# Performance work log

Measured on AMD Instinct MI355X. Metric: run time of the kernel, lower is better.

Reference implementation:

```python
import jax, jax.numpy as jnp
import numpy as np

N_NODES = 100000
N_EDGES = 800000
D_IN = 512
D_OUT = 512


def setup_inputs() -> dict:
    key = jax.random.key(0)
    ks = jax.random.split(key, 6)
    std = 1.0 / np.sqrt(D_OUT)
    return {
        "x": jax.random.normal(ks[0], (N_NODES, D_IN), dtype=jnp.float32),
        "adj_row": jax.random.randint(ks[1], (N_EDGES,), 0, N_NODES, dtype=jnp.int32),
        "adj_col": jax.random.randint(ks[2], (N_EDGES,), 0, N_NODES, dtype=jnp.int32),
        "adj_vals": jax.random.uniform(ks[3], (N_EDGES,), dtype=jnp.float32),
        "weight": jax.random.uniform(ks[4], (D_IN, D_OUT), minval=-std, maxval=std, dtype=jnp.float32),
        "b": jax.random.uniform(ks[5], (D_OUT,), minval=-std, maxval=std, dtype=jnp.float32),
    }


def reference(x, adj_row, adj_col, adj_vals, weight, b):
    # support = X W  : dense GEMM [N, D_in] x [D_in, D_out]
    support = jnp.matmul(x, weight)
    # output = A @ support + b, A given as COO (row, col, vals)
    gathered = adj_vals[:, None] * support[adj_col]  # [E, D_out]
    out = jax.ops.segment_sum(gathered, adj_row, num_segments=N_NODES)
    return out + b
```

## Files before the change

### kernel.cpp

```cpp
#include <hip/hip_runtime.h>
#include <hip/hip_bf16.h>
#include <stdint.h>

#define D 512
#define D4 (D / 4)
#define SB 256
#define CHUNK 256

typedef __bf16 bf16x8 __attribute__((ext_vector_type(8)));
typedef float  f32x4  __attribute__((ext_vector_type(4)));

__device__ __forceinline__ unsigned short f2bf(float f) {
    uint32_t u = __float_as_uint(f);
    uint32_t r = u + 0x7fffu + ((u >> 16) & 1u);
    return (unsigned short)(r >> 16);
}

__device__ __forceinline__ uint32_t pack2(float lo, float hi) {
    return (uint32_t)f2bf(lo) | ((uint32_t)f2bf(hi) << 16);
}

__device__ __forceinline__ float bflo(uint32_t p) {
    return __uint_as_float((p & 0x0000ffffu) << 16);
}
__device__ __forceinline__ float bfhi(uint32_t p) {
    return __uint_as_float(p & 0xffff0000u);
}

__global__ __launch_bounds__(256) void cvt_x_kernel(const float4* __restrict__ x,
                                                    uint4* __restrict__ xb,
                                                    long n8) {
    long i = (long)blockIdx.x * 256 + threadIdx.x;
    if (i >= n8) return;
    float4 a = x[i * 2];
    float4 b = x[i * 2 + 1];
    uint4 o;
    o.x = pack2(a.x, a.y);
    o.y = pack2(a.z, a.w);
    o.z = pack2(b.x, b.y);
    o.w = pack2(b.z, b.w);
    xb[i] = o;
}

__global__ __launch_bounds__(256) void cvt_w_kernel(const float* __restrict__ w,
                                                    unsigned short* __restrict__ wt) {
    __shared__ float t[32][33];
    const int tx = threadIdx.x & 31;
    const int ty = threadIdx.x >> 5;
    const int n0 = blockIdx.x * 32;
    const int k0 = blockIdx.y * 32;
#pragma unroll
    for (int i = 0; i < 4; ++i)
        t[ty + i * 8][tx] = w[(long)(k0 + ty + i * 8) * D + n0 + tx];
    __syncthreads();
#pragma unroll
    for (int i = 0; i < 4; ++i)
        wt[(long)(n0 + ty + i * 8) * D + k0 + tx] = f2bf(t[tx][ty + i * 8]);
}

__global__ __launch_bounds__(256) void zero_kernel(int* __restrict__ p, int n) {
    int i = blockIdx.x * 256 + threadIdx.x;
    if (i < n) p[i] = 0;
}

__global__ __launch_bounds__(256) void hist_kernel(const int* __restrict__ erow,
                                                   int* __restrict__ cnt, int nE) {
    int i = blockIdx.x * 256 + threadIdx.x;
    int stride = gridDim.x * 256;
    for (; i < nE; i += stride) atomicAdd(&cnt[erow[i]], 1);
}

__global__ __launch_bounds__(256) void scan_part_kernel(const int* __restrict__ cnt,
                                                        int* __restrict__ bsum, int M) {
    const int b = blockIdx.x;
    const int chunk = (M + SB - 1) / SB;
    const int lo = b * chunk;
    const int hi = min(M, lo + chunk);
    int s = 0;
    for (int i = lo + (int)threadIdx.x; i < hi; i += 256) s += cnt[i];
#pragma unroll
    for (int off = 32; off; off >>= 1) s += __shfl_down(s, off);
    __shared__ int ws[4];
    const int wv = threadIdx.x >> 6;
    if ((threadIdx.x & 63) == 0) ws[wv] = s;
    __syncthreads();
    if (threadIdx.x == 0) bsum[b] = ws[0] + ws[1] + ws[2] + ws[3];
}

__global__ __launch_bounds__(SB) void scan_base_kernel(const int* __restrict__ bsum,
                                                       int* __restrict__ bbase,
                                                       int* __restrict__ rowptr, int M) {
    const int tid  = (int)threadIdx.x;
    const int lane = tid & 63;
    const int wv   = tid >> 6;
    const int v = bsum[tid];
    int s = v;
#pragma unroll
    for (int off = 1; off < 64; off <<= 1) {
        int t = __shfl_up(s, off);
        if (lane >= off) s += t;
    }
    __shared__ int wsum[4];
    if (lane == 63) wsum[wv] = s;
    __syncthreads();
    int wb = 0;
    for (int j = 0; j < wv; ++j) wb += wsum[j];
    bbase[tid] = wb + s - v;
    if (tid == SB - 1) rowptr[M] = wb + s;
}

__global__ __launch_bounds__(256) void scan_final_kernel(const int* __restrict__ cnt,
                                                         const int* __restrict__ bbase,
                                                         int* __restrict__ rowptr,
                                                         int* __restrict__ heads, int M) {
    const int b = blockIdx.x;
    const int chunk = (M + SB - 1) / SB;
    const int lo = b * chunk;
    const int hi = min(M, lo + chunk);
    const int lane = threadIdx.x & 63;
    const int wv   = threadIdx.x >> 6;
    __shared__ int wsum[4];
    __shared__ int s_carry;
    if (threadIdx.x == 0) s_carry = bbase[b];
    __syncthreads();
    for (int base = lo; base < hi; base += 256) {
        const int i = base + (int)threadIdx.x;
        const int v = (i < hi) ? cnt[i] : 0;
        int s = v;
#pragma unroll
        for (int off = 1; off < 64; off <<= 1) {
            int t = __shfl_up(s, off);
            if (lane >= off) s += t;
        }
        if (lane == 63) wsum[wv] = s;
        __syncthreads();
        int wb = s_carry;
        for (int j = 0; j < wv; ++j) wb += wsum[j];
        const int excl = wb + s - v;
        if (i < hi) { rowptr[i] = excl; heads[i] = excl; }
        __syncthreads();
        if (threadIdx.x == 0) s_carry += wsum[0] + wsum[1] + wsum[2] + wsum[3];
        __syncthreads();
    }
}

__global__ __launch_bounds__(256) void edge_sort_kernel(const int* __restrict__ erow,
                                                        const int* __restrict__ ecol,
                                                        const float* __restrict__ eval,
                                                        int* __restrict__ heads,
                                                        int* __restrict__ scol,
                                                        float* __restrict__ sval,
                                                        int nE) {
    int i = blockIdx.x * 256 + threadIdx.x;
    int stride = gridDim.x * 256;
    for (; i < nE; i += stride) {
        const int r = erow[i];
        const int p = atomicAdd(&heads[r], 1);
        scol[p] = ecol[i];
        sval[p] = eval[i];
    }
}

__global__ __launch_bounds__(256) void gemm_kernel(const unsigned short* __restrict__ Xb,
                                                   const unsigned short* __restrict__ Wt,
                                                   unsigned short* __restrict__ Sup,
                                                   int M) {
    __shared__ __align__(16) unsigned short As[128 * 64];
    __shared__ __align__(16) unsigned short Bs[128 * 64];
    const int tid  = threadIdx.x;
    const int wv   = tid >> 6;
    const int lane = tid & 63;
    const int tileM = blockIdx.x * 128;
    const int tileN = blockIdx.y * 128;
    const int wm = wv >> 1, wn = wv & 1;

    f32x4 acc[4][4];
#pragma unroll
    for (int i = 0; i < 4; ++i)
#pragma unroll
        for (int j = 0; j < 4; ++j) acc[i][j] = (f32x4)0.0f;

    const int srow = lane >> 3;
    const int sgrn = (lane & 7) ^ srow;
    const int scol = sgrn * 8;

    const int fm  = lane & 15;
    const int fkq = lane >> 4;

    for (int kt = 0; kt < D; kt += 64) {
        __syncthreads();
#pragma unroll
        for (int i = 0; i < 4; ++i) {
            const int c   = wv * 4 + i;
            const int row = c * 8 + srow;
            int rg = tileM + row;
            rg = (rg < M) ? rg : (M - 1);
            const unsigned short* ga = Xb + (long)rg * D + kt + scol;
            __builtin_amdgcn_global_load_lds(
                (const __attribute__((address_space(1))) void*)ga,
                (__attribute__((address_space(3))) void*)(As + c * 512), 16, 0, 0);
            const unsigned short* gb = Wt + (long)(tileN + row) * D + kt + scol;
            __builtin_amdgcn_global_load_lds(
                (const __attribute__((address_space(1))) void*)gb,
                (__attribute__((address_space(3))) void*)(Bs + c * 512), 16, 0, 0);
        }
        __syncthreads();
#pragma unroll
        for (int kk = 0; kk < 2; ++kk) {
            bf16x8 af[4], bfr[4];
#pragma unroll
            for (int mi = 0; mi < 4; ++mi) {
                const int m = wm * 64 + mi * 16 + fm;
                const int g = (kk * 4 + fkq) ^ (m & 7);
                af[mi] = *(const bf16x8*)(As + m * 64 + g * 8);
            }
#pragma unroll
            for (int ni = 0; ni < 4; ++ni) {
                const int n = wn * 64 + ni * 16 + fm;
                const int g = (kk * 4 + fkq) ^ (n & 7);
                bfr[ni] = *(const bf16x8*)(Bs + n * 64 + g * 8);
            }
#pragma unroll
            for (int mi = 0; mi < 4; ++mi)
#pragma unroll
                for (int ni = 0; ni < 4; ++ni)
                    acc[mi][ni] = __builtin_amdgcn_mfma_f32_16x16x32_bf16(
                        af[mi], bfr[ni], acc[mi][ni], 0, 0, 0);
        }
    }

    const int colb = tileN + wn * 64 + fm;
#pragma unroll
    for (int mi = 0; mi < 4; ++mi) {
        const int rb = tileM + wm * 64 + mi * 16 + fkq * 4;
#pragma unroll
        for (int r = 0; r < 4; ++r) {
            const int row = rb + r;
            if (row < M) {
                unsigned short* dst = Sup + (long)row * D + colb;
#pragma unroll
                for (int ni = 0; ni < 4; ++ni)
                    dst[ni * 16] = f2bf(acc[mi][ni][r]);
            }
        }
    }
}

__global__ __launch_bounds__(256) void aggregate_kernel(const unsigned short* __restrict__ sup,
                                                        const int* __restrict__ rowptr,
                                                        const int* __restrict__ scol,
                                                        const float* __restrict__ sval,
                                                        const float* __restrict__ bias,
                                                        float* __restrict__ out,
                                                        int M, int c0) {
    const int lane = threadIdx.x & 63;
    const int row  = (int)((blockIdx.x * 256 + threadIdx.x) >> 6);
    if (row >= M) return;
    int e = rowptr[row];
    const int end = rowptr[row + 1];

    const float4 b0 = *(const float4*)(bias + c0 + lane * 4);
    float acc[4] = {b0.x, b0.y, b0.z, b0.w};

    const unsigned short* supc = sup + c0 + lane * 4;

    for (; e + 4 <= end; e += 4) {
        const int cc0 = scol[e + 0], cc1 = scol[e + 1];
        const int cc2 = scol[e + 2], cc3 = scol[e + 3];
        const float v0 = sval[e + 0], v1 = sval[e + 1];
        const float v2 = sval[e + 2], v3 = sval[e + 3];
        const uint2 p0 = *(const uint2*)(supc + (long)cc0 * D);
        const uint2 p1 = *(const uint2*)(supc + (long)cc1 * D);
        const uint2 p2 = *(const uint2*)(supc + (long)cc2 * D);
        const uint2 p3 = *(const uint2*)(supc + (long)cc3 * D);
        acc[0] += v0 * bflo(p0.x); acc[1] += v0 * bfhi(p0.x);
        acc[2] += v0 * bflo(p0.y); acc[3] += v0 * bfhi(p0.y);
        acc[0] += v1 * bflo(p1.x); acc[1] += v1 * bfhi(p1.x);
        acc[2] += v1 * bflo(p1.y); acc[3] += v1 * bfhi(p1.y);
        acc[0] += v2 * bflo(p2.x); acc[1] += v2 * bfhi(p2.x);
        acc[2] += v2 * bflo(p2.y); acc[3] += v2 * bfhi(p2.y);
        acc[0] += v3 * bflo(p3.x); acc[1] += v3 * bfhi(p3.x);
        acc[2] += v3 * bflo(p3.y); acc[3] += v3 * bfhi(p3.y);
    }
    for (; e + 2 <= end; e += 2) {
        const int cc0 = scol[e + 0], cc1 = scol[e + 1];
        const float v0 = sval[e + 0], v1 = sval[e + 1];
        const uint2 p0 = *(const uint2*)(supc + (long)cc0 * D);
        const uint2 p1 = *(const uint2*)(supc + (long)cc1 * D);
        acc[0] += v0 * bflo(p0.x); acc[1] += v0 * bfhi(p0.x);
        acc[2] += v0 * bflo(p0.y); acc[3] += v0 * bfhi(p0.y);
        acc[0] += v1 * bflo(p1.x); acc[1] += v1 * bfhi(p1.x);
        acc[2] += v1 * bflo(p1.y); acc[3] += v1 * bfhi(p1.y);
    }
    for (; e < end; ++e) {
        const int cc = scol[e];
        const float v = sval[e];
        const uint2 p = *(const uint2*)(supc + (long)cc * D);
        acc[0] += v * bflo(p.x); acc[1] += v * bfhi(p.x);
        acc[2] += v * bflo(p.y); acc[3] += v * bfhi(p.y);
    }

    *(float4*)(out + (long)row * D + c0 + lane * 4) =
        (float4){acc[0], acc[1], acc[2], acc[3]};
}

extern "C" void kernel_launch(void* const* d_in, const int* in_sizes, int n_in,
                              void* d_out, int out_size, void* d_ws, size_t ws_size,
                              hipStream_t stream) {
    const float* x        = (const float*)d_in[0];
    const int*   adj_row  = (const int*)d_in[1];
    const int*   adj_col  = (const int*)d_in[2];
    const float* adj_vals = (const float*)d_in[3];
    const float* weight   = (const float*)d_in[4];
    const float* bias     = (const float*)d_in[5];
    float* out = (float*)d_out;

    const int M = in_sizes[0] / D;
    const int E = in_sizes[1];

    char* ws = (char*)d_ws;
    size_t off = 0;
    unsigned short* Xb  = (unsigned short*)(ws + off); off += (size_t)M * D * 2;
    unsigned short* Sup = (unsigned short*)(ws + off); off += (size_t)M * D * 2;
    unsigned short* Wt  = (unsigned short*)(ws + off); off += (size_t)D * D * 2;
    int*   rowptr = (int*)(ws + off);   off += (size_t)(M + 1) * 4;
    int*   heads  = (int*)(ws + off);   off += (size_t)M * 4;
    int*   scol   = (int*)(ws + off);   off += (size_t)E * 4;
    float* sval   = (float*)(ws + off); off += (size_t)E * 4;
    int*   bsum   = (int*)(ws + off);   off += (size_t)SB * 4;
    int*   bbase  = (int*)(ws + off);   off += (size_t)SB * 4;
    int* cnt = heads;

    zero_kernel<<<(M + 255) / 256, 256, 0, stream>>>(cnt, M);
    hist_kernel<<<1024, 256, 0, stream>>>(adj_row, cnt, E);
    scan_part_kernel<<<SB, 256, 0, stream>>>(cnt, bsum, M);
    scan_base_kernel<<<1, SB, 0, stream>>>(bsum, bbase, rowptr, M);
    scan_final_kernel<<<SB, 256, 0, stream>>>(cnt, bbase, rowptr, heads, M);
    edge_sort_kernel<<<1024, 256, 0, stream>>>(adj_row, adj_col, adj_vals,
                                               heads, scol, sval, E);

    {
        long n8 = (long)M * D / 8;
        cvt_x_kernel<<<(int)((n8 + 255) / 256), 256, 0, stream>>>(
            (const float4*)x, (uint4*)Xb, n8);
    }
    cvt_w_kernel<<<dim3(D / 32, D / 32), 256, 0, stream>>>(weight, Wt);
    gemm_kernel<<<dim3((M + 127) / 128, D / 128), 256, 0, stream>>>(Xb, Wt, Sup, M);

    aggregate_kernel<<<(M * 64 + 255) / 256, 256, 0, stream>>>(
        Sup, rowptr, scol, sval, bias, out, M, 0);
    aggregate_kernel<<<(M * 64 + 255) / 256, 256, 0, stream>>>(
        Sup, rowptr, scol, sval, bias, out, M, CHUNK);
}
```

Measured before the change: 649.0 us.

## Fuse fp32-to-bf16 X conversion into GEMM with full-width N tiles

Removes the separate X conversion kernel and its bf16 workspace buffer. The GEMM now reads fp32 X directly, converts it to bf16 in registers and stores it to LDS. Each block covers 64 rows and all 512 output columns with 8 waves, so X is read once instead of once per N tile. This cuts a full write and read of the converted X, but the A-tile path is now synchronous register loads rather than direct global-to-LDS loads, and each block holds a larger B tile in LDS (64 KB), which limits occupancy.

```diff
diff --git a/kernel.cpp b/kernel.cpp
--- a/kernel.cpp
+++ b/kernel.cpp
@@ -3,9 +3,9 @@
 #include <stdint.h>
 
 #define D 512
-#define D4 (D / 4)
 #define SB 256
 #define CHUNK 256
+#define BM 64
 
 typedef __bf16 bf16x8 __attribute__((ext_vector_type(8)));
 typedef float  f32x4  __attribute__((ext_vector_type(4)));
@@ -25,21 +25,6 @@
 }
 __device__ __forceinline__ float bfhi(uint32_t p) {
     return __uint_as_float(p & 0xffff0000u);
-}
-
-__global__ __launch_bounds__(256) void cvt_x_kernel(const float4* __restrict__ x,
-                                                    uint4* __restrict__ xb,
-                                                    long n8) {
-    long i = (long)blockIdx.x * 256 + threadIdx.x;
-    if (i >= n8) return;
-    float4 a = x[i * 2];
-    float4 b = x[i * 2 + 1];
-    uint4 o;
-    o.x = pack2(a.x, a.y);
-    o.y = pack2(a.z, a.w);
-    o.z = pack2(b.x, b.y);
-    o.w = pack2(b.z, b.w);
-    xb[i] = o;
 }
 
 __global__ __launch_bounds__(256) void cvt_w_kernel(const float* __restrict__ w,
@@ -161,18 +146,16 @@
     }
 }
 
-__global__ __launch_bounds__(256) void gemm_kernel(const unsigned short* __restrict__ Xb,
-                                                   const unsigned short* __restrict__ Wt,
-                                                   unsigned short* __restrict__ Sup,
-                                                   int M) {
-    __shared__ __align__(16) unsigned short As[128 * 64];
-    __shared__ __align__(16) unsigned short Bs[128 * 64];
+__global__ __launch_bounds__(512, 4) void gemm_kernel(const float* __restrict__ X,
+                                                      const unsigned short* __restrict__ Wt,
+                                                      unsigned short* __restrict__ Sup,
+                                                      int M) {
+    __shared__ __align__(16) unsigned short As[BM * 64];
+    __shared__ __align__(16) unsigned short Bs[512 * 64];
     const int tid  = threadIdx.x;
     const int wv   = tid >> 6;
     const int lane = tid & 63;
-    const int tileM = blockIdx.x * 128;
-    const int tileN = blockIdx.y * 128;
-    const int wm = wv >> 1, wn = wv & 1;
+    const int tileM = blockIdx.x * BM;
 
     f32x4 acc[4][4];
 #pragma unroll
@@ -187,19 +170,28 @@
     const int fm  = lane & 15;
     const int fkq = lane >> 4;
 
+    int arow = tileM + wv * 8 + srow;
+    arow = (arow < M) ? arow : (M - 1);
+    const float* agbase = X + (long)arow * D + scol;
+
     for (int kt = 0; kt < D; kt += 64) {
         __syncthreads();
-#pragma unroll
-        for (int i = 0; i < 4; ++i) {
-            const int c   = wv * 4 + i;
+        {
+            const float* gx = agbase + kt;
+            const float4 a = *(const float4*)gx;
+            const float4 b = *(const float4*)(gx + 4);
+            uint4 o;
+            o.x = pack2(a.x, a.y);
+            o.y = pack2(a.z, a.w);
+            o.z = pack2(b.x, b.y);
+            o.w = pack2(b.z, b.w);
+            *(uint4*)(As + wv * 512 + lane * 8) = o;
+        }
+#pragma unroll
+        for (int i = 0; i < 8; ++i) {
+            const int c   = wv * 8 + i;
             const int row = c * 8 + srow;
-            int rg = tileM + row;
-            rg = (rg < M) ? rg : (M - 1);
-            const unsigned short* ga = Xb + (long)rg * D + kt + scol;
-            __builtin_amdgcn_global_load_lds(
-                (const __attribute__((address_space(1))) void*)ga,
-                (__attribute__((address_space(3))) void*)(As + c * 512), 16, 0, 0);
-            const unsigned short* gb = Wt + (long)(tileN + row) * D + kt + scol;
+            const unsigned short* gb = Wt + (long)row * D + kt + scol;
             __builtin_amdgcn_global_load_lds(
                 (const __attribute__((address_space(1))) void*)gb,
                 (__attribute__((address_space(3))) void*)(Bs + c * 512), 16, 0, 0);
@@ -210,13 +202,13 @@
             bf16x8 af[4], bfr[4];
 #pragma unroll
             for (int mi = 0; mi < 4; ++mi) {
-                const int m = wm * 64 + mi * 16 + fm;
+                const int m = mi * 16 + fm;
                 const int g = (kk * 4 + fkq) ^ (m & 7);
                 af[mi] = *(const bf16x8*)(As + m * 64 + g * 8);
             }
 #pragma unroll
             for (int ni = 0; ni < 4; ++ni) {
-                const int n = wn * 64 + ni * 16 + fm;
+                const int n = wv * 64 + ni * 16 + fm;
                 const int g = (kk * 4 + fkq) ^ (n & 7);
                 bfr[ni] = *(const bf16x8*)(Bs + n * 64 + g * 8);
             }
@@ -229,10 +221,10 @@
         }
     }
 
-    const int colb = tileN + wn * 64 + fm;
+    const int colb = wv * 64 + fm;
 #pragma unroll
     for (int mi = 0; mi < 4; ++mi) {
-        const int rb = tileM + wm * 64 + mi * 16 + fkq * 4;
+        const int rb = tileM + mi * 16 + fkq * 4;
 #pragma unroll
         for (int r = 0; r < 4; ++r) {
             const int row = rb + r;
@@ -320,7 +312,6 @@
 
     char* ws = (char*)d_ws;
     size_t off = 0;
-    unsigned short* Xb  = (unsigned short*)(ws + off); off += (size_t)M * D * 2;
     unsigned short* Sup = (unsigned short*)(ws + off); off += (size_t)M * D * 2;
     unsigned short* Wt  = (unsigned short*)(ws + off); off += (size_t)D * D * 2;
     int*   rowptr = (int*)(ws + off);   off += (size_t)(M + 1) * 4;
@@ -339,13 +330,8 @@
     edge_sort_kernel<<<1024, 256, 0, stream>>>(adj_row, adj_col, adj_vals,
                                                heads, scol, sval, E);
 
-    {
-        long n8 = (long)M * D / 8;
-        cvt_x_kernel<<<(int)((n8 + 255) / 256), 256, 0, stream>>>(
-            (const float4*)x, (uint4*)Xb, n8);
-    }
     cvt_w_kernel<<<dim3(D / 32, D / 32), 256, 0, stream>>>(weight, Wt);
-    gemm_kernel<<<dim3((M + 127) / 128, D / 128), 256, 0, stream>>>(Xb, Wt, Sup, M);
+    gemm_kernel<<<(M + BM - 1) / BM, 512, 0, stream>>>(x, Wt, Sup, M);
 
     aggregate_kernel<<<(M * 64 + 255) / 256, 256, 0, stream>>>(
         Sup, rowptr, scol, sval, bias, out, M, 0);
```

Result: faster. 609.4 us (-6.1%).
